# Kernel tuning notes

Measured on AMD Instinct MI355X. Metric: run time of the kernel, lower is better.

Reference implementation:

```python
import jax, jax.numpy as jnp
import numpy as np

B, H, W, C = 4, 256, 256, 256
WS = 8          # window size (both dims)
HEADS = 1
SEQ = WS * WS   # 64 tokens per window
NW = B * (H // WS) * (W // WS)  # 4096 windows
INNER = C * HEADS


def setup_inputs() -> dict:
    key = jax.random.key(0)
    k1, k2, k3, k4 = jax.random.split(key, 4)
    x = jax.random.normal(k1, (B, H, W, C), dtype=jnp.float32)
    attn = jax.random.uniform(k2, (NW, HEADS, SEQ, SEQ), dtype=jnp.float32)
    # to_v: Linear(dim, inner_dim, bias=False); stored as [in, out] for x @ Wv
    Wv = jax.random.normal(k3, (C, INNER), dtype=jnp.float32) * (C ** -0.5)
    # to_out: Linear(inner_dim, dim)
    Wo = jax.random.normal(k4, (INNER, C), dtype=jnp.float32) * (INNER ** -0.5)
    bo = jnp.zeros((C,), dtype=jnp.float32)
    return {"x": x, "attn": attn, "Wv": Wv, "Wo": Wo, "bo": bo}


def reference(x, attn, Wv, Wo, bo):
    b, h, w, c = x.shape
    nh, nw = h // WS, w // WS
    # window partition: b (h b0) (w b1) c -> (b h w) (b0 b1) c
    xw = x.reshape(b, nh, WS, nw, WS, c).transpose(0, 1, 3, 2, 4, 5)
    xw = xw.reshape(b * nh * nw, SEQ, c)
    # value projection, split heads: n s (h d) -> n h s d
    v = (xw @ Wv).reshape(-1, SEQ, HEADS, c).transpose(0, 2, 1, 3)
    # precomputed-attention weighted sum
    out = jnp.einsum('nhij,nhjd->nhid', attn, v)
    # merge heads: n h s d -> n s (h d)
    out = out.transpose(0, 2, 1, 3).reshape(-1, SEQ, HEADS * c)
    out = out @ Wo + bo
    # window un-partition: (b h w) (b0 b1) c -> b (h b0) (w b1) c
    out = out.reshape(b, nh, nw, WS, WS, c).transpose(0, 1, 3, 2, 4, 5)
    return out.reshape(b, h, w, c)
```

## Files before the change

kernel.cpp:

```cpp
#include <hip/hip_runtime.h>
#include <hip/hip_bf16.h>


typedef __bf16 bf16x8 __attribute__((ext_vector_type(8)));
typedef __bf16 bf16x4 __attribute__((ext_vector_type(4)));
typedef float  f32x16 __attribute__((ext_vector_type(16)));
typedef float  f32x4  __attribute__((ext_vector_type(4)));

#define MFMA32(a, b, c) __builtin_amdgcn_mfma_f32_32x32x16_bf16(a, b, c, 0, 0, 0)

__global__ void wfuse_kernel(const float* __restrict__ Wv,
                             const float* __restrict__ Wo,
                             __bf16* __restrict__ WT) {
  const int n = blockIdx.x;
  const int k = threadIdx.x;
  const float* wvrow = Wv + k * 256;
  float acc = 0.f;
#pragma unroll 4
  for (int j = 0; j < 256; j += 4) {
    f32x4 wv = *(const f32x4*)(wvrow + j);
    acc += wv.x * Wo[(j + 0) * 256 + n];
    acc += wv.y * Wo[(j + 1) * 256 + n];
    acc += wv.z * Wo[(j + 2) * 256 + n];
    acc += wv.w * Wo[(j + 3) * 256 + n];
  }
  WT[n * 256 + k] = (__bf16)acc;
}

__global__ __launch_bounds__(512, 8)
void na_msa_kernel(const float* __restrict__ x,
                   const float* __restrict__ attn,
                   const __bf16* __restrict__ WT,
                   const float* __restrict__ bo,
                   float* __restrict__ out) {
  __shared__ char lds[40960];
  char* lds_xw = lds;
  char* lds_at = lds + 32768;

  const int t    = threadIdx.x;
  const int lane = t & 63;
  const int wv   = t >> 6;
  const int ln31 = lane & 31;
  const int lh   = lane >> 5;

  const int n  = blockIdx.x;
  const int wi = n & 31;
  const int hi = (n >> 5) & 31;
  const int b  = n >> 10;
  const long base = (((long)(b * 256 + hi * 8)) * 256 + wi * 8) * 256;
  const float* xp = x + base;

#pragma unroll
  for (int i = 0; i < 8; ++i) {
    int gi = i * 512 + t;
    int rowblk = gi >> 9;
    int f = gi & 511;
    f32x4 v = *(const f32x4*)(xp + rowblk * 65536 + f * 4);
    int tok = rowblk * 8 + (f >> 6);
    int ch0 = (f & 63) * 4;
    bf16x4 hv = { (__bf16)v.x, (__bf16)v.y, (__bf16)v.z, (__bf16)v.w };
    int byt = tok * 512 + ((ch0 * 2) ^ ((tok & 31) << 4));
    *(bf16x4*)(lds_xw + byt) = hv;
  }

  const float* ap = attn + (long)n * 4096;
#pragma unroll
  for (int i = 0; i < 2; ++i) {
    int fi = i * 512 + t;
    f32x4 v = *(const f32x4*)(ap + fi * 4);
    int row = fi >> 4;
    int k0 = (fi & 15) * 4;
    bf16x4 hv = { (__bf16)v.x, (__bf16)v.y, (__bf16)v.z, (__bf16)v.w };
    int byt = row * 128 + ((k0 * 2) ^ ((row & 7) << 4));
    *(bf16x4*)(lds_at + byt) = hv;
  }
  __syncthreads();

  f32x16 acc0 = {}, acc1 = {};
  const __bf16* wtp = WT + (wv * 32 + ln31) * 256 + 8 * lh;
#pragma unroll
  for (int ks = 0; ks < 16; ++ks) {
    int kk = ks * 16 + 8 * lh;
    int byt0 = ln31 * 512 + ((kk * 2) ^ (ln31 << 4));
    bf16x8 a0 = *(const bf16x8*)(lds_xw + byt0);
    bf16x8 a1 = *(const bf16x8*)(lds_xw + byt0 + 16384);
    bf16x8 b0 = *(const bf16x8*)(wtp + ks * 16);
    acc0 = MFMA32(a0, b0, acc0);
    acc1 = MFMA32(a1, b0, acc1);
  }
  __syncthreads();

  char* ztw = lds + (wv << 12);
  {
    int rb = ln31 * 128;
    int sw = (ln31 & 7) << 4;
#pragma unroll
    for (int g = 0; g < 4; ++g) {
      int tok0 = g * 8 + 4 * lh;
      bf16x4 h0 = { (__bf16)acc0[4 * g + 0], (__bf16)acc0[4 * g + 1],
                    (__bf16)acc0[4 * g + 2], (__bf16)acc0[4 * g + 3] };
      *(bf16x4*)(ztw + rb + ((tok0 * 2) ^ sw)) = h0;
      int tok1 = 32 + g * 8 + 4 * lh;
      bf16x4 h1 = { (__bf16)acc1[4 * g + 0], (__bf16)acc1[4 * g + 1],
                    (__bf16)acc1[4 * g + 2], (__bf16)acc1[4 * g + 3] };
      *(bf16x4*)(ztw + rb + ((tok1 * 2) ^ sw)) = h1;
    }
  }

  f32x16 o0 = {}, o1 = {};
#pragma unroll
  for (int ks = 0; ks < 4; ++ks) {
    int kk = ks * 16 + 8 * lh;
    int ab0 = ln31 * 128 + ((kk * 2) ^ ((ln31 & 7) << 4));
    bf16x8 a0 = *(const bf16x8*)(lds_at + ab0);
    bf16x8 a1 = *(const bf16x8*)(lds_at + ab0 + 4096);
    bf16x8 b0 = *(const bf16x8*)(ztw + ab0);
    o0 = MFMA32(a0, b0, o0);
    o1 = MFMA32(a1, b0, o1);
  }

  float* op = out + base;
  const int ch = wv * 32 + ln31;
  const float bv = bo[ch];
#pragma unroll
  for (int r = 0; r < 16; ++r) {
    int tok = (r & 3) + 8 * (r >> 2) + 4 * lh;
    op[(tok >> 3) * 65536 + (tok & 7) * 256 + ch] = o0[r] + bv;
  }
#pragma unroll
  for (int r = 0; r < 16; ++r) {
    int tok = 32 + (r & 3) + 8 * (r >> 2) + 4 * lh;
    op[(tok >> 3) * 65536 + (tok & 7) * 256 + ch] = o1[r] + bv;
  }
}

extern "C" void kernel_launch(void* const* d_in, const int* in_sizes, int n_in,
                              void* d_out, int out_size, void* d_ws, size_t ws_size,
                              hipStream_t stream) {
  const float* x    = (const float*)d_in[0];
  const float* attn = (const float*)d_in[1];
  const float* Wv   = (const float*)d_in[2];
  const float* Wo   = (const float*)d_in[3];
  const float* bo   = (const float*)d_in[4];
  float* out = (float*)d_out;
  __bf16* WT = (__bf16*)d_ws;

  wfuse_kernel<<<256, 256, 0, stream>>>(Wv, Wo, WT);
  na_msa_kernel<<<4096, 512, 0, stream>>>(x, attn, WT, bo, out);
}
```

Baseline: 176.4 us.

## Make kernel persistent over 8 windows with double-buffered LDS prefetch and shuffle-built B fragments

Each block now handles 8 consecutive windows rather than one. The next window's x and attn tiles are loaded into registers while the current window's MFMAs run, then written to a second LDS buffer. The intermediate projection no longer round-trips through LDS; B-operand fragments for the attention MFMA are built in registers with cross-half-wave shuffles, which removes one barrier per window. The cost is 80KB of LDS, lower occupancy (launch bounds 4), and only 512 blocks, which may underfill the 256 CUs or balance poorly.

```diff
diff --git a/kernel.cpp b/kernel.cpp
--- a/kernel.cpp
+++ b/kernel.cpp
@@ -6,6 +6,8 @@
 typedef __bf16 bf16x4 __attribute__((ext_vector_type(4)));
 typedef float  f32x16 __attribute__((ext_vector_type(16)));
 typedef float  f32x4  __attribute__((ext_vector_type(4)));
+typedef unsigned int uint;
+typedef uint   uint4v __attribute__((ext_vector_type(4)));
 
 #define MFMA32(a, b, c) __builtin_amdgcn_mfma_f32_32x32x16_bf16(a, b, c, 0, 0, 0)
 
@@ -27,110 +29,185 @@
   WT[n * 256 + k] = (__bf16)acc;
 }
 
-__global__ __launch_bounds__(512, 8)
+static __device__ __forceinline__ uint pkbf(float lo, float hi) {
+  return (uint)__builtin_bit_cast(unsigned short, (__bf16)lo) |
+         ((uint)__builtin_bit_cast(unsigned short, (__bf16)hi) << 16);
+}
+
+static __device__ __forceinline__ void build_bfrags(const f32x16 acc, int lh,
+                                                    bf16x8* bf) {
+  uint wd[8];
+#pragma unroll
+  for (int g = 0; g < 4; ++g) {
+    wd[2 * g]     = pkbf(acc[4 * g + 0], acc[4 * g + 1]);
+    wd[2 * g + 1] = pkbf(acc[4 * g + 2], acc[4 * g + 3]);
+  }
+#pragma unroll
+  for (int s = 0; s < 2; ++s) {
+    uint o0 = (uint)__shfl_xor((int)wd[4 * s + 2], 32);
+    uint o1 = (uint)__shfl_xor((int)wd[4 * s + 3], 32);
+    uint o2 = (uint)__shfl_xor((int)wd[4 * s + 0], 32);
+    uint o3 = (uint)__shfl_xor((int)wd[4 * s + 1], 32);
+    uint w0 = lh ? o0 : wd[4 * s + 0];
+    uint w1 = lh ? o1 : wd[4 * s + 1];
+    uint w2 = lh ? wd[4 * s + 2] : o2;
+    uint w3 = lh ? wd[4 * s + 3] : o3;
+    uint4v uv = { w0, w1, w2, w3 };
+    bf[s] = __builtin_bit_cast(bf16x8, uv);
+  }
+}
+
+__global__ __launch_bounds__(512, 4)
 void na_msa_kernel(const float* __restrict__ x,
                    const float* __restrict__ attn,
                    const __bf16* __restrict__ WT,
                    const float* __restrict__ bo,
                    float* __restrict__ out) {
-  __shared__ char lds[40960];
-  char* lds_xw = lds;
-  char* lds_at = lds + 32768;
+  __shared__ char lds[81920];
 
   const int t    = threadIdx.x;
   const int lane = t & 63;
-  const int wv   = t >> 6;
+  const int wvi  = t >> 6;
   const int ln31 = lane & 31;
   const int lh   = lane >> 5;
 
-  const int n  = blockIdx.x;
-  const int wi = n & 31;
-  const int hi = (n >> 5) & 31;
-  const int b  = n >> 10;
-  const long base = (((long)(b * 256 + hi * 8)) * 256 + wi * 8) * 256;
-  const float* xp = x + base;
-
-#pragma unroll
+  const __bf16* wtp = WT + (wvi * 32 + ln31) * 256 + 8 * lh;
+  const float bv = bo[wvi * 32 + ln31];
+
+  const int w0 = blockIdx.x * 8;
+
+  {
+    const int w = w0;
+    const long base = (((long)(((w >> 10) * 256) + ((w >> 5) & 31) * 8)) * 256 +
+                       (w & 31) * 8) * 256;
+    const float* xp = x + base;
+    const float* ap = attn + (long)w * 4096;
+#pragma unroll
+    for (int j = 0; j < 8; ++j) {
+      int gi = j * 512 + t;
+      int rowblk = gi >> 9, f = gi & 511;
+      f32x4 v = *(const f32x4*)(xp + rowblk * 65536 + f * 4);
+      int tok = rowblk * 8 + (f >> 6);
+      int ch0 = (f & 63) * 4;
+      bf16x4 hv = { (__bf16)v.x, (__bf16)v.y, (__bf16)v.z, (__bf16)v.w };
+      *(bf16x4*)(lds + tok * 512 + ((ch0 * 2) ^ ((tok & 31) << 4))) = hv;
+    }
+#pragma unroll
+    for (int j = 0; j < 2; ++j) {
+      int fi = j * 512 + t;
+      f32x4 v = *(const f32x4*)(ap + fi * 4);
+      int row = fi >> 4, k0 = (fi & 15) * 4;
+      bf16x4 hv = { (__bf16)v.x, (__bf16)v.y, (__bf16)v.z, (__bf16)v.w };
+      *(bf16x4*)(lds + 32768 + row * 128 + ((k0 * 2) ^ ((row & 7) << 4))) = hv;
+    }
+  }
+  asm volatile("s_waitcnt lgkmcnt(0)" ::: "memory");
+  __builtin_amdgcn_s_barrier();
+  __builtin_amdgcn_sched_barrier(0);
+
+  int cur = 0;
   for (int i = 0; i < 8; ++i) {
-    int gi = i * 512 + t;
-    int rowblk = gi >> 9;
-    int f = gi & 511;
-    f32x4 v = *(const f32x4*)(xp + rowblk * 65536 + f * 4);
-    int tok = rowblk * 8 + (f >> 6);
-    int ch0 = (f & 63) * 4;
-    bf16x4 hv = { (__bf16)v.x, (__bf16)v.y, (__bf16)v.z, (__bf16)v.w };
-    int byt = tok * 512 + ((ch0 * 2) ^ ((tok & 31) << 4));
-    *(bf16x4*)(lds_xw + byt) = hv;
-  }
-
-  const float* ap = attn + (long)n * 4096;
-#pragma unroll
-  for (int i = 0; i < 2; ++i) {
-    int fi = i * 512 + t;
-    f32x4 v = *(const f32x4*)(ap + fi * 4);
-    int row = fi >> 4;
-    int k0 = (fi & 15) * 4;
-    bf16x4 hv = { (__bf16)v.x, (__bf16)v.y, (__bf16)v.z, (__bf16)v.w };
-    int byt = row * 128 + ((k0 * 2) ^ ((row & 7) << 4));
-    *(bf16x4*)(lds_at + byt) = hv;
-  }
-  __syncthreads();
-
-  f32x16 acc0 = {}, acc1 = {};
-  const __bf16* wtp = WT + (wv * 32 + ln31) * 256 + 8 * lh;
-#pragma unroll
-  for (int ks = 0; ks < 16; ++ks) {
-    int kk = ks * 16 + 8 * lh;
-    int byt0 = ln31 * 512 + ((kk * 2) ^ (ln31 << 4));
-    bf16x8 a0 = *(const bf16x8*)(lds_xw + byt0);
-    bf16x8 a1 = *(const bf16x8*)(lds_xw + byt0 + 16384);
-    bf16x8 b0 = *(const bf16x8*)(wtp + ks * 16);
-    acc0 = MFMA32(a0, b0, acc0);
-    acc1 = MFMA32(a1, b0, acc1);
-  }
-  __syncthreads();
-
-  char* ztw = lds + (wv << 12);
-  {
-    int rb = ln31 * 128;
-    int sw = (ln31 & 7) << 4;
-#pragma unroll
-    for (int g = 0; g < 4; ++g) {
-      int tok0 = g * 8 + 4 * lh;
-      bf16x4 h0 = { (__bf16)acc0[4 * g + 0], (__bf16)acc0[4 * g + 1],
-                    (__bf16)acc0[4 * g + 2], (__bf16)acc0[4 * g + 3] };
-      *(bf16x4*)(ztw + rb + ((tok0 * 2) ^ sw)) = h0;
-      int tok1 = 32 + g * 8 + 4 * lh;
-      bf16x4 h1 = { (__bf16)acc1[4 * g + 0], (__bf16)acc1[4 * g + 1],
-                    (__bf16)acc1[4 * g + 2], (__bf16)acc1[4 * g + 3] };
-      *(bf16x4*)(ztw + rb + ((tok1 * 2) ^ sw)) = h1;
-    }
-  }
-
-  f32x16 o0 = {}, o1 = {};
-#pragma unroll
-  for (int ks = 0; ks < 4; ++ks) {
-    int kk = ks * 16 + 8 * lh;
-    int ab0 = ln31 * 128 + ((kk * 2) ^ ((ln31 & 7) << 4));
-    bf16x8 a0 = *(const bf16x8*)(lds_at + ab0);
-    bf16x8 a1 = *(const bf16x8*)(lds_at + ab0 + 4096);
-    bf16x8 b0 = *(const bf16x8*)(ztw + ab0);
-    o0 = MFMA32(a0, b0, o0);
-    o1 = MFMA32(a1, b0, o1);
-  }
-
-  float* op = out + base;
-  const int ch = wv * 32 + ln31;
-  const float bv = bo[ch];
-#pragma unroll
-  for (int r = 0; r < 16; ++r) {
-    int tok = (r & 3) + 8 * (r >> 2) + 4 * lh;
-    op[(tok >> 3) * 65536 + (tok & 7) * 256 + ch] = o0[r] + bv;
-  }
-#pragma unroll
-  for (int r = 0; r < 16; ++r) {
-    int tok = 32 + (r & 3) + 8 * (r >> 2) + 4 * lh;
-    op[(tok >> 3) * 65536 + (tok & 7) * 256 + ch] = o1[r] + bv;
+    const int w = w0 + i;
+    char* lds_xw = lds + cur * 40960;
+    char* lds_at = lds_xw + 32768;
+
+    f32x4 px0, px1, px2, px3, px4, px5, px6, px7, pa0, pa1;
+    if (i < 7) {
+      const int wn = w + 1;
+      const long nb = (((long)(((wn >> 10) * 256) + ((wn >> 5) & 31) * 8)) * 256 +
+                       (wn & 31) * 8) * 256;
+      const float* xp = x + nb;
+      const float* ap = attn + (long)wn * 4096;
+      {
+        int gi;
+        gi = 0 * 512 + t; px0 = *(const f32x4*)(xp + (gi >> 9) * 65536 + (gi & 511) * 4);
+        gi = 1 * 512 + t; px1 = *(const f32x4*)(xp + (gi >> 9) * 65536 + (gi & 511) * 4);
+        gi = 2 * 512 + t; px2 = *(const f32x4*)(xp + (gi >> 9) * 65536 + (gi & 511) * 4);
+        gi = 3 * 512 + t; px3 = *(const f32x4*)(xp + (gi >> 9) * 65536 + (gi & 511) * 4);
+        gi = 4 * 512 + t; px4 = *(const f32x4*)(xp + (gi >> 9) * 65536 + (gi & 511) * 4);
+        gi = 5 * 512 + t; px5 = *(const f32x4*)(xp + (gi >> 9) * 65536 + (gi & 511) * 4);
+        gi = 6 * 512 + t; px6 = *(const f32x4*)(xp + (gi >> 9) * 65536 + (gi & 511) * 4);
+        gi = 7 * 512 + t; px7 = *(const f32x4*)(xp + (gi >> 9) * 65536 + (gi & 511) * 4);
+        pa0 = *(const f32x4*)(ap + (0 * 512 + t) * 4);
+        pa1 = *(const f32x4*)(ap + (1 * 512 + t) * 4);
+      }
+      __builtin_amdgcn_sched_barrier(0);
+    }
+
+    f32x16 acc0 = {}, acc1 = {};
+#pragma unroll 4
+    for (int ks = 0; ks < 16; ++ks) {
+      int kk = ks * 16 + 8 * lh;
+      int byt0 = ln31 * 512 + ((kk * 2) ^ (ln31 << 4));
+      bf16x8 a0 = *(const bf16x8*)(lds_xw + byt0);
+      bf16x8 a1 = *(const bf16x8*)(lds_xw + byt0 + 16384);
+      bf16x8 b0 = *(const bf16x8*)(wtp + ks * 16);
+      acc0 = MFMA32(a0, b0, acc0);
+      acc1 = MFMA32(a1, b0, acc1);
+    }
+
+    bf16x8 bfr[4];
+    build_bfrags(acc0, lh, &bfr[0]);
+    build_bfrags(acc1, lh, &bfr[2]);
+
+    if (i < 7) {
+      char* bxw = lds + (cur ^ 1) * 40960;
+      char* bat = bxw + 32768;
+      f32x4 pxa[8] = { px0, px1, px2, px3, px4, px5, px6, px7 };
+#pragma unroll
+      for (int j = 0; j < 8; ++j) {
+        int gi = j * 512 + t;
+        int rowblk = gi >> 9, f = gi & 511;
+        int tok = rowblk * 8 + (f >> 6);
+        int ch0 = (f & 63) * 4;
+        f32x4 v = pxa[j];
+        bf16x4 hv = { (__bf16)v.x, (__bf16)v.y, (__bf16)v.z, (__bf16)v.w };
+        *(bf16x4*)(bxw + tok * 512 + ((ch0 * 2) ^ ((tok & 31) << 4))) = hv;
+      }
+      {
+        int fi = 0 * 512 + t;
+        int row = fi >> 4, k0 = (fi & 15) * 4;
+        bf16x4 hv = { (__bf16)pa0.x, (__bf16)pa0.y, (__bf16)pa0.z, (__bf16)pa0.w };
+        *(bf16x4*)(bat + row * 128 + ((k0 * 2) ^ ((row & 7) << 4))) = hv;
+        fi = 1 * 512 + t;
+        row = fi >> 4; k0 = (fi & 15) * 4;
+        bf16x4 hv1 = { (__bf16)pa1.x, (__bf16)pa1.y, (__bf16)pa1.z, (__bf16)pa1.w };
+        *(bf16x4*)(bat + row * 128 + ((k0 * 2) ^ ((row & 7) << 4))) = hv1;
+      }
+    }
+
+    f32x16 o0 = {}, o1 = {};
+#pragma unroll
+    for (int ks = 0; ks < 4; ++ks) {
+      int kk = ks * 16 + 8 * lh;
+      int ab0 = ln31 * 128 + ((kk * 2) ^ ((ln31 & 7) << 4));
+      bf16x8 a0 = *(const bf16x8*)(lds_at + ab0);
+      bf16x8 a1 = *(const bf16x8*)(lds_at + ab0 + 4096);
+      o0 = MFMA32(a0, bfr[ks], o0);
+      o1 = MFMA32(a1, bfr[ks], o1);
+    }
+
+    {
+      const long base = (((long)(((w >> 10) * 256) + ((w >> 5) & 31) * 8)) * 256 +
+                         (w & 31) * 8) * 256;
+      float* op = out + base;
+      const int ch = wvi * 32 + ln31;
+#pragma unroll
+      for (int r = 0; r < 16; ++r) {
+        int tok = (r & 3) + 8 * (r >> 2) + 4 * lh;
+        op[(tok >> 3) * 65536 + (tok & 7) * 256 + ch] = o0[r] + bv;
+      }
+#pragma unroll
+      for (int r = 0; r < 16; ++r) {
+        int tok = 32 + (r & 3) + 8 * (r >> 2) + 4 * lh;
+        op[(tok >> 3) * 65536 + (tok & 7) * 256 + ch] = o1[r] + bv;
+      }
+    }
+
+    asm volatile("s_waitcnt lgkmcnt(0)" ::: "memory");
+    __builtin_amdgcn_s_barrier();
+    __builtin_amdgcn_sched_barrier(0);
+    cur ^= 1;
   }
 }
 
@@ -146,5 +223,5 @@
   __bf16* WT = (__bf16*)d_ws;
 
   wfuse_kernel<<<256, 256, 0, stream>>>(Wv, Wo, WT);
-  na_msa_kernel<<<4096, 512, 0, stream>>>(x, attn, WT, bo, out);
-}
+  na_msa_kernel<<<512, 512, 0, stream>>>(x, attn, WT, bo, out);
+}
```

After: 221.2 us. 25.4% more time.
